# Kernel tuning notes

Hardware: AMD Instinct MI355X
Metric: run time of the kernel (lower is better)

## Reference

```python
import jax, jax.numpy as jnp
import numpy as np

B, D, NS, C, H = 4096, 1024, 16000, 1000, 256


def setup_inputs() -> dict:
    key = jax.random.key(0)
    ks = jax.random.split(key, 8)
    # L2-normalized image features (output of frozen CLIP encode_image + norm)
    q = jax.random.normal(ks[0], (B, D), jnp.float32)
    q = q / jnp.linalg.norm(q, axis=-1, keepdims=True)
    # zero-shot CLIP logits
    z = jax.random.normal(ks[1], (B, C), jnp.float32)
    # L2-normalized support/cache features
    keys = jax.random.normal(ks[2], (NS, D), jnp.float32)
    keys = keys / jnp.linalg.norm(keys, axis=-1, keepdims=True)
    # one-hot support labels
    labels = jax.random.randint(ks[3], (NS,), 0, C)
    values = jax.nn.one_hot(labels, C, dtype=jnp.float32)
    # gate MLP params (small init like nn.Linear default scale)
    fc1_w = jax.random.normal(ks[4], (H, D), jnp.float32) * 0.02
    fc1_b = jnp.zeros((H,), jnp.float32)
    fc2_w = jax.random.normal(ks[5], (2, H), jnp.float32) * 0.02
    fc2_b = jnp.zeros((2,), jnp.float32)
    post_scale = jnp.ones((1,), jnp.float32)
    return {"q": q, "z": z, "keys": keys, "values": values,
            "fc1_w": fc1_w, "fc1_b": fc1_b, "fc2_w": fc2_w, "fc2_b": fc2_b,
            "post_scale": post_scale}


def reference(q, z, keys, values, fc1_w, fc1_b, fc2_w, fc2_b, post_scale):
    # GateMLP: per-image alpha in (0,1), beta > 0
    x = jax.nn.relu(q @ fc1_w.T + fc1_b)            # [B, H]
    g = x @ fc2_w.T + fc2_b                          # [B, 2]
    alpha_hat = jax.nn.sigmoid(g[:, 0:1])            # [B, 1]
    beta = jax.nn.softplus(g[:, 1:2]) + 0.001        # [B, 1] (learn_beta=True)
    # cache logits: sim -> exp affinity -> label aggregation
    sim = q @ keys.T                                 # [B, Ns]
    affinity = jnp.exp(beta * sim)                   # [B, Ns]
    c = affinity @ values                            # [B, C]
    # gated convex fusion with zero-shot logits
    logits = ((1.0 - alpha_hat) * z + alpha_hat * c) * post_scale
    return (logits, alpha_hat, beta)
```

## Files before the change

kernel.cpp:

```cpp
#include <hip/hip_runtime.h>
#include <hip/hip_bf16.h>
#include <stdint.h>

#define B_  4096
#define D_  1024
#define NS_ 16000
#define C_  1000
#define H_  256
#define LBLK 4000
#define QCB  1024
#define KCB  4000
#define FCB  64
#define CONVB (QCB + KCB + FCB)
#define RSTRIDE 2048

typedef __attribute__((ext_vector_type(8))) short bf16x8;
typedef __attribute__((ext_vector_type(4))) float f32x4;
typedef __attribute__((ext_vector_type(16))) float f32x16;
typedef __attribute__((ext_vector_type(8))) int i32x8;

__device__ __forceinline__ unsigned short f2bf(float f) {
  union { float f; unsigned u; } v; v.f = f;
  unsigned u = v.u;
  u += 0x7FFF + ((u >> 16) & 1);
  return (unsigned short)(u >> 16);
}

__device__ __forceinline__ float bf2f(unsigned short h) {
  union { unsigned u; float f; } v; v.u = ((unsigned)h) << 16;
  return v.f;
}

__global__ void prep_kernel(const float4* __restrict__ q, const float4* __restrict__ keys,
                            const float4* __restrict__ fc1, const float* __restrict__ values,
                            ushort4* __restrict__ qb, int* __restrict__ q8,
                            int* __restrict__ keys8, ushort4* __restrict__ fc1b,
                            int* __restrict__ labels, int* __restrict__ hist) {
  const int bid = blockIdx.x;
  if (bid < QCB) {
    const size_t i0 = (size_t)bid * 1024 + threadIdx.x;
    #pragma unroll
    for (int k = 0; k < 4; ++k) {
      const size_t i = i0 + k * 256;
      float4 v = q[i];
      ushort4 r; r.x = f2bf(v.x); r.y = f2bf(v.y); r.z = f2bf(v.z); r.w = f2bf(v.w);
      qb[i] = r;
      int p = __builtin_amdgcn_cvt_pk_fp8_f32(v.x * 64.f, v.y * 64.f, 0, false);
      p     = __builtin_amdgcn_cvt_pk_fp8_f32(v.z * 64.f, v.w * 64.f, p, true);
      q8[i] = p;
    }
    return;
  }
  if (bid < QCB + KCB) {
    const size_t i0 = (size_t)(bid - QCB) * 1024 + threadIdx.x;
    #pragma unroll
    for (int k = 0; k < 4; ++k) {
      const size_t i = i0 + k * 256;
      float4 v = keys[i];
      int p = __builtin_amdgcn_cvt_pk_fp8_f32(v.x * 64.f, v.y * 64.f, 0, false);
      p     = __builtin_amdgcn_cvt_pk_fp8_f32(v.z * 64.f, v.w * 64.f, p, true);
      keys8[i] = p;
    }
    return;
  }
  if (bid < CONVB) {
    const size_t i0 = (size_t)(bid - QCB - KCB) * 1024 + threadIdx.x;
    #pragma unroll
    for (int k = 0; k < 4; ++k) {
      const size_t i = i0 + k * 256;
      float4 v = fc1[i];
      ushort4 r; r.x = f2bf(v.x); r.y = f2bf(v.y); r.z = f2bf(v.z); r.w = f2bf(v.w);
      fc1b[i] = r;
    }
    return;
  }
  const int s = (bid - CONVB) * 4 + (threadIdx.x >> 6);
  const int lane = threadIdx.x & 63;
  const float4* row = (const float4*)(values + (size_t)s * C_);
  int lab = -1;
  for (int j = lane; j < C_ / 4; j += 64) {
    float4 v = row[j];
    if (v.x > 0.5f) lab = j * 4 + 0;
    if (v.y > 0.5f) lab = j * 4 + 1;
    if (v.z > 0.5f) lab = j * 4 + 2;
    if (v.w > 0.5f) lab = j * 4 + 3;
    if (__ballot(lab >= 0)) break;
  }
  if (lab >= 0) { labels[s] = lab; atomicAdd(&hist[lab], 1); }
}

__global__ __launch_bounds__(1024) void sortpipe_kernel(
    const int* __restrict__ hist, const int* __restrict__ labels,
    int* __restrict__ sortidx, int* __restrict__ runid, int* __restrict__ labstart)
{
  __shared__ int sscan[1024];
  __shared__ int sboff[C_ + 1];
  __shared__ int scnt[C_];
  __shared__ unsigned short slab[NS_];
  __shared__ int stile[NS_ / 128];
  const int t = threadIdx.x;

  int v = (t < C_) ? hist[t] : 0;
  sscan[t] = v;
  if (t < C_) scnt[t] = 0;
  __syncthreads();
  for (int off = 1; off < 1024; off <<= 1) {
    int u = (t >= off) ? sscan[t - off] : 0;
    __syncthreads(); sscan[t] += u; __syncthreads();
  }
  if (t == 0) sboff[0] = 0;
  if (t < C_) sboff[t + 1] = sscan[t];
  __syncthreads();

  for (int s = t; s < NS_; s += 1024) {
    const int lab = labels[s];
    const int pos = sboff[lab] + atomicAdd(&scnt[lab], 1);
    sortidx[pos] = s;
    slab[pos] = (unsigned short)lab;
  }
  __syncthreads();

  const int c0 = t * 16;
  int flags[16]; int cnt = 0;
  if (c0 < NS_) {
    int prev = (c0 == 0) ? slab[0] : slab[c0 - 1];
    #pragma unroll
    for (int i = 0; i < 16; ++i) {
      const int l = slab[c0 + i];
      const int f = ((c0 + i) != 0) && (l != prev);
      flags[i] = f; cnt += f; prev = l;
    }
  }
  sscan[t] = cnt; __syncthreads();
  for (int off = 1; off < 1024; off <<= 1) {
    int u = (t >= off) ? sscan[t - off] : 0;
    __syncthreads(); sscan[t] += u; __syncthreads();
  }
  if (c0 < NS_ && (t & 7) == 0) stile[t >> 3] = (sscan[t] - cnt) + flags[0];
  __syncthreads();
  if (c0 < NS_) {
    int run = sscan[t] - cnt;
    const int base = (c0 >> 7) * 16 - stile[c0 >> 7];
    #pragma unroll
    for (int i = 0; i < 16; ++i) {
      run += flags[i];
      runid[c0 + i] = base + run;
    }
  }
  if (t == 0) runid[NS_] = (NS_ >> 7) * 16;
  __threadfence();
  __syncthreads();
  if (t <= C_) labstart[t] = runid[sboff[t]];
}

__global__ __launch_bounds__(256, 2) void gemmgate_kernel(
    const short* __restrict__ A, const short* __restrict__ Bm,
    const float* __restrict__ bias, const float* __restrict__ fc2_w,
    const float* __restrict__ fc2_b, float* __restrict__ ab)
{
  __shared__ short As[32 * 64];
  __shared__ short Bs[256 * 64];
  __shared__ float gred[4][32][2];

  const int tid  = threadIdx.x;
  const int wave = tid >> 6, lane = tid & 63;
  const int quad = lane >> 4, l16 = lane & 15;
  const int wn = wave;
  const int rstart = blockIdx.x * 32;

  f32x4 acc[2][4];
  #pragma unroll
  for (int i = 0; i < 2; ++i)
    #pragma unroll
    for (int j = 0; j < 4; ++j) acc[i][j] = (f32x4)0.f;

  const int r_  = (lane >> 3);
  const int kc_ = ((lane & 7) ^ r_) * 8;

  for (int kt = 0; kt < D_; kt += 64) {
    __syncthreads();
    {
      const int row = wave * 8 + r_;
      const short* gA = A + (size_t)(rstart + row) * D_ + kt + kc_;
      __builtin_amdgcn_global_load_lds(
          (const __attribute__((address_space(1))) void*)gA,
          (__attribute__((address_space(3))) void*)(As + wave * 512), 16, 0, 0);
    }
    #pragma unroll
    for (int i = 0; i < 8; ++i) {
      const int g = i * 4 + wave;
      const int row = g * 8 + r_;
      const short* gB = Bm + (size_t)row * D_ + kt + kc_;
      __builtin_amdgcn_global_load_lds(
          (const __attribute__((address_space(1))) void*)gB,
          (__attribute__((address_space(3))) void*)(Bs + g * 512), 16, 0, 0);
    }
    __syncthreads();
    #pragma unroll
    for (int ks = 0; ks < 64; ks += 32) {
      bf16x8 af[2], bfr[4];
      const int kb = (ks >> 3) + quad;
      #pragma unroll
      for (int mt = 0; mt < 2; ++mt) {
        const int row = mt * 16 + l16;
        af[mt] = *(const bf16x8*)(As + row * 64 + ((kb ^ (row & 7)) << 3));
      }
      #pragma unroll
      for (int nt = 0; nt < 4; ++nt) {
        const int row = wn * 64 + nt * 16 + l16;
        bfr[nt] = *(const bf16x8*)(Bs + row * 64 + ((kb ^ (row & 7)) << 3));
      }
      #pragma unroll
      for (int mt = 0; mt < 2; ++mt)
        #pragma unroll
        for (int nt = 0; nt < 4; ++nt)
          acc[mt][nt] = __builtin_amdgcn_mfma_f32_16x16x32_bf16(af[mt], bfr[nt], acc[mt][nt], 0, 0, 0);
    }
  }

  float g0p[2][4], g1p[2][4];
  #pragma unroll
  for (int mt = 0; mt < 2; ++mt)
    #pragma unroll
    for (int r = 0; r < 4; ++r) { g0p[mt][r] = 0.f; g1p[mt][r] = 0.f; }
  #pragma unroll
  for (int nt = 0; nt < 4; ++nt) {
    const int col = wn * 64 + nt * 16 + l16;
    const float bv = bias[col];
    const float w0 = fc2_w[col], w1 = fc2_w[H_ + col];
    #pragma unroll
    for (int mt = 0; mt < 2; ++mt)
      #pragma unroll
      for (int r = 0; r < 4; ++r) {
        float xv = acc[mt][nt][r] + bv;
        xv = xv > 0.f ? xv : 0.f;
        g0p[mt][r] += xv * w0;
        g1p[mt][r] += xv * w1;
      }
  }
  #pragma unroll
  for (int mt = 0; mt < 2; ++mt)
    #pragma unroll
    for (int r = 0; r < 4; ++r) {
      float a0 = g0p[mt][r], a1 = g1p[mt][r];
      #pragma unroll
      for (int off = 8; off > 0; off >>= 1) {
        a0 += __shfl_xor(a0, off);
        a1 += __shfl_xor(a1, off);
      }
      if (l16 == 0) {
        const int row = mt * 16 + quad * 4 + r;
        gred[wave][row][0] = a0;
        gred[wave][row][1] = a1;
      }
    }
  __syncthreads();
  if (tid < 32) {
    float g0 = gred[0][tid][0] + gred[1][tid][0] + gred[2][tid][0] + gred[3][tid][0] + fc2_b[0];
    float g1 = gred[0][tid][1] + gred[1][tid][1] + gred[2][tid][1] + gred[3][tid][1] + fc2_b[1];
    ab[rstart + tid]      = 1.f / (1.f + __expf(-g0));
    ab[B_ + rstart + tid] = fmaxf(g1, 0.f) + log1pf(__expf(-fabsf(g1))) + 0.001f;
  }
}

__device__ __forceinline__ i32x8 mx_frag(const char* base, int lrow, int kh, int sel) {
  const int c0 = kh * 4 + sel * 2;
  const int s = lrow & 7;
  const int4 lo = *(const int4*)(base + lrow * 128 + (((c0    ) ^ s) << 4));
  const int4 hi = *(const int4*)(base + lrow * 128 + (((c0 + 1) ^ s) << 4));
  i32x8 f;
  f[0] = lo.x; f[1] = lo.y; f[2] = lo.z; f[3] = lo.w;
  f[4] = hi.x; f[5] = hi.y; f[6] = hi.z; f[7] = hi.w;
  return f;
}

__global__ __launch_bounds__(256, 2) void mxgemm_kernel(
    const char* __restrict__ A8, const char* __restrict__ B8,
    const float* __restrict__ beta, float* __restrict__ partials,
    const int* __restrict__ sortidx, const int* __restrict__ runid)
{
  __shared__ __align__(16) char smem[32768];
  __shared__ float sbeta[128];
  __shared__ __align__(16) unsigned short Es[16 * 136];
  char* As = smem;
  char* Bs = smem + 16384;

  const int tid  = threadIdx.x;
  const int wave = tid >> 6, lane = tid & 63;
  const int sel  = lane >> 5, l32 = lane & 31;
  const int wm = wave >> 1, wn = wave & 1;

  const int sb  = (blockIdx.x & 7) * 500 + (blockIdx.x >> 3);
  const int rstart = (sb & 31) * 128;
  const int nstart = (sb >> 5) * 128;

  for (int i = tid; i < (16 * 136) / 2; i += 256) ((int*)Es)[i] = 0;
  if (tid < 128) sbeta[tid] = beta[rstart + tid];
  __syncthreads();
  if (tid < 128) Es[(runid[nstart + tid] & 15) * 136 + tid] = 0x3F80;

  const int srow_ = (lane >> 3);
  const int gch_  = (lane & 7) ^ srow_;

  int arow[4], brow[4];
  #pragma unroll
  for (int i = 0; i < 4; ++i) {
    const int row = wave * 32 + i * 8 + srow_;
    arow[i] = rstart + row;
    brow[i] = sortidx[nstart + row];
  }

  f32x16 acc[2][2];
  #pragma unroll
  for (int i = 0; i < 2; ++i)
    #pragma unroll
    for (int j = 0; j < 2; ++j) acc[i][j] = (f32x16)0.f;

  for (int kt = 0; kt < D_; kt += 128) {
    __syncthreads();
    #pragma unroll
    for (int i = 0; i < 4; ++i) {
      const char* gA = A8 + (size_t)arow[i] * D_ + kt + (gch_ << 4);
      const char* gB = B8 + (size_t)brow[i] * D_ + kt + (gch_ << 4);
      __builtin_amdgcn_global_load_lds(
          (const __attribute__((address_space(1))) void*)gA,
          (__attribute__((address_space(3))) void*)(As + wave * 4096 + i * 1024), 16, 0, 0);
      __builtin_amdgcn_global_load_lds(
          (const __attribute__((address_space(1))) void*)gB,
          (__attribute__((address_space(3))) void*)(Bs + wave * 4096 + i * 1024), 16, 0, 0);
    }
    __syncthreads();
    #pragma unroll
    for (int kh = 0; kh < 2; ++kh) {
      i32x8 a0 = mx_frag(As, wm * 64 +  0 + l32, kh, sel);
      i32x8 a1 = mx_frag(As, wm * 64 + 32 + l32, kh, sel);
      i32x8 b0 = mx_frag(Bs, wn * 64 +  0 + l32, kh, sel);
      i32x8 b1 = mx_frag(Bs, wn * 64 + 32 + l32, kh, sel);
      acc[0][0] = __builtin_amdgcn_mfma_scale_f32_32x32x64_f8f6f4(a0, b0, acc[0][0], 0, 0, 0, 121, 0, 121);
      acc[0][1] = __builtin_amdgcn_mfma_scale_f32_32x32x64_f8f6f4(a0, b1, acc[0][1], 0, 0, 0, 121, 0, 121);
      acc[1][0] = __builtin_amdgcn_mfma_scale_f32_32x32x64_f8f6f4(a1, b0, acc[1][0], 0, 0, 0, 121, 0, 121);
      acc[1][1] = __builtin_amdgcn_mfma_scale_f32_32x32x64_f8f6f4(a1, b1, acc[1][1], 0, 0, 0, 121, 0, 121);
    }
  }

  __syncthreads();
  unsigned short* tile = (unsigned short*)smem;
  #pragma unroll
  for (int mt = 0; mt < 2; ++mt) {
    #pragma unroll
    for (int nt = 0; nt < 2; ++nt) {
      const int col = wn * 64 + nt * 32 + l32;
      const int cc = col >> 3, cl = col & 7;
      #pragma unroll
      for (int r = 0; r < 16; ++r) {
        const int row = wm * 64 + mt * 32 + (r & 3) + 8 * (r >> 2) + 4 * sel;
        const float v = __expf(sbeta[row] * acc[mt][nt][r]);
        tile[row * 128 + (((cc ^ (row & 7)) << 3) | cl)] = f2bf(v);
      }
    }
  }
  __syncthreads();

  {
    const int quad = lane >> 4, l16 = lane & 15;
    const int rowb = wave * 32;
    f32x4 racc[2];
    racc[0] = (f32x4)0.f; racc[1] = (f32x4)0.f;
    #pragma unroll
    for (int kc = 0; kc < 4; ++kc) {
      const bf16x8 bfrag = *(const bf16x8*)(Es + l16 * 136 + kc * 32 + quad * 8);
      #pragma unroll
      for (int rg = 0; rg < 2; ++rg) {
        const int row = rowb + rg * 16 + l16;
        const int kch = kc * 4 + quad;
        const bf16x8 afrag = *(const bf16x8*)(tile + row * 128 + ((kch ^ (row & 7)) << 3));
        racc[rg] = __builtin_amdgcn_mfma_f32_16x16x32_bf16(afrag, bfrag, racc[rg], 0, 0, 0);
      }
    }
    const int tb = (nstart >> 7) * 16;
    #pragma unroll
    for (int rg = 0; rg < 2; ++rg) {
      #pragma unroll
      for (int r = 0; r < 4; ++r) {
        const int row = rowb + rg * 16 + quad * 4 + r;
        partials[(size_t)(rstart + row) * RSTRIDE + tb + l16] = racc[rg][r];
      }
    }
  }
}

__global__ __launch_bounds__(256) void reduce_kernel(
    const float* __restrict__ partials, const int* __restrict__ labstart,
    const float* __restrict__ z, const float* __restrict__ ps, float* __restrict__ out) {
  __shared__ __align__(16) float sp[RSTRIDE];
  __shared__ int sls[C_ + 1];
  const int b = blockIdx.x;
  const int t = threadIdx.x;
  for (int i = t; i <= C_; i += 256) sls[i] = labstart[i];
  const float4* p4 = (const float4*)(partials + (size_t)b * RSTRIDE);
  float4* s4 = (float4*)sp;
  for (int i = t; i < RSTRIDE / 4; i += 256) s4[i] = p4[i];
  __syncthreads();
  const float a  = out[(size_t)B_ * C_ + b];
  const float sc = ps[0];
  for (int lab = t; lab < C_; lab += 256) {
    float c = 0.f;
    for (int j = sls[lab]; j < sls[lab + 1]; ++j) c += sp[j];
    const size_t oi = (size_t)b * C_ + lab;
    out[oi] = ((1.f - a) * z[oi] + a * c) * sc;
  }
}

extern "C" void kernel_launch(void* const* d_in, const int* in_sizes, int n_in,
                              void* d_out, int out_size, void* d_ws, size_t ws_size,
                              hipStream_t stream) {
  const float* q          = (const float*)d_in[0];
  const float* z          = (const float*)d_in[1];
  const float* keys       = (const float*)d_in[2];
  const float* values     = (const float*)d_in[3];
  const float* fc1_w      = (const float*)d_in[4];
  const float* fc1_b      = (const float*)d_in[5];
  const float* fc2_w      = (const float*)d_in[6];
  const float* fc2_b      = (const float*)d_in[7];
  const float* post_scale = (const float*)d_in[8];
  float* out = (float*)d_out;

  char* ws = (char*)d_ws;
  short* qb        = (short*)(ws);
  char*  q8        = (char*) (ws +  8388608);
  char*  keys8     = (char*) (ws + 12582912);
  short* fc1b      = (short*)(ws + 28966912);
  int*   labels    = (int*)  (ws + 29491200);
  int*   hist      = (int*)  (ws + 33749504);
  int*   sortidx   = (int*)  (ws + 33761792);
  int*   runid     = (int*)  (ws + 33889792);
  int*   labstart  = (int*)  (ws + 33953808);
  float* partials  = (float*)(ws + 33959936);

  float* alpha = out + (size_t)B_ * C_;
  float* beta  = alpha + B_;

  hipMemsetAsync(hist, 0, 4096, stream);

  prep_kernel<<<CONVB + LBLK, 256, 0, stream>>>(
      (const float4*)q, (const float4*)keys, (const float4*)fc1_w, values,
      (ushort4*)qb, (int*)q8, (int*)keys8, (ushort4*)fc1b, labels, hist);

  sortpipe_kernel<<<1, 1024, 0, stream>>>(hist, labels, sortidx, runid, labstart);

  gemmgate_kernel<<<B_ / 32, 256, 0, stream>>>(qb, fc1b, fc1_b, fc2_w, fc2_b, alpha);

  mxgemm_kernel<<<4000, 256, 0, stream>>>(
      q8, keys8, beta, partials, sortidx, runid);

  reduce_kernel<<<B_, 256, 0, stream>>>(partials, labstart, z, post_scale, out);
}
```

Baseline: 324.3 us.

## Double-buffer LDS tiles in MX-FP8 GEMM and use a 2D grid

```diff
diff --git a/kernel.cpp b/kernel.cpp
--- a/kernel.cpp
+++ b/kernel.cpp
@@ -279,20 +279,16 @@
     const float* __restrict__ beta, float* __restrict__ partials,
     const int* __restrict__ sortidx, const int* __restrict__ runid)
 {
-  __shared__ __align__(16) char smem[32768];
+  __shared__ __align__(16) char smem[65536];
   __shared__ float sbeta[128];
   __shared__ __align__(16) unsigned short Es[16 * 136];
-  char* As = smem;
-  char* Bs = smem + 16384;
 
   const int tid  = threadIdx.x;
   const int wave = tid >> 6, lane = tid & 63;
   const int sel  = lane >> 5, l32 = lane & 31;
   const int wm = wave >> 1, wn = wave & 1;
-
-  const int sb  = (blockIdx.x & 7) * 500 + (blockIdx.x >> 3);
-  const int rstart = (sb & 31) * 128;
-  const int nstart = (sb >> 5) * 128;
+  const int rstart = blockIdx.x * 128;
+  const int nstart = blockIdx.y * 128;
 
   for (int i = tid; i < (16 * 136) / 2; i += 256) ((int*)Es)[i] = 0;
   if (tid < 128) sbeta[tid] = beta[rstart + tid];
@@ -316,34 +312,60 @@
     #pragma unroll
     for (int j = 0; j < 2; ++j) acc[i][j] = (f32x16)0.f;
 
-  for (int kt = 0; kt < D_; kt += 128) {
-    __syncthreads();
-    #pragma unroll
-    for (int i = 0; i < 4; ++i) {
-      const char* gA = A8 + (size_t)arow[i] * D_ + kt + (gch_ << 4);
-      const char* gB = B8 + (size_t)brow[i] * D_ + kt + (gch_ << 4);
-      __builtin_amdgcn_global_load_lds(
-          (const __attribute__((address_space(1))) void*)gA,
-          (__attribute__((address_space(3))) void*)(As + wave * 4096 + i * 1024), 16, 0, 0);
-      __builtin_amdgcn_global_load_lds(
-          (const __attribute__((address_space(1))) void*)gB,
-          (__attribute__((address_space(3))) void*)(Bs + wave * 4096 + i * 1024), 16, 0, 0);
-    }
-    __syncthreads();
-    #pragma unroll
-    for (int kh = 0; kh < 2; ++kh) {
-      i32x8 a0 = mx_frag(As, wm * 64 +  0 + l32, kh, sel);
-      i32x8 a1 = mx_frag(As, wm * 64 + 32 + l32, kh, sel);
-      i32x8 b0 = mx_frag(Bs, wn * 64 +  0 + l32, kh, sel);
-      i32x8 b1 = mx_frag(Bs, wn * 64 + 32 + l32, kh, sel);
-      acc[0][0] = __builtin_amdgcn_mfma_scale_f32_32x32x64_f8f6f4(a0, b0, acc[0][0], 0, 0, 0, 121, 0, 121);
-      acc[0][1] = __builtin_amdgcn_mfma_scale_f32_32x32x64_f8f6f4(a0, b1, acc[0][1], 0, 0, 0, 121, 0, 121);
-      acc[1][0] = __builtin_amdgcn_mfma_scale_f32_32x32x64_f8f6f4(a1, b0, acc[1][0], 0, 0, 0, 121, 0, 121);
-      acc[1][1] = __builtin_amdgcn_mfma_scale_f32_32x32x64_f8f6f4(a1, b1, acc[1][1], 0, 0, 0, 121, 0, 121);
-    }
-  }
-
-  __syncthreads();
+  __syncthreads();
+
+#define STAGE(BUF, KT)                                                              \
+  {                                                                                 \
+    char* As_ = smem + (BUF) * 32768;                                               \
+    char* Bs_ = As_ + 16384;                                                        \
+    _Pragma("unroll")                                                               \
+    for (int i = 0; i < 4; ++i) {                                                   \
+      const char* gA = A8 + (size_t)arow[i] * D_ + (KT) + (gch_ << 4);              \
+      const char* gB = B8 + (size_t)brow[i] * D_ + (KT) + (gch_ << 4);              \
+      __builtin_amdgcn_global_load_lds(                                             \
+          (const __attribute__((address_space(1))) void*)gA,                        \
+          (__attribute__((address_space(3))) void*)(As_ + wave * 4096 + i * 1024),  \
+          16, 0, 0);                                                                \
+      __builtin_amdgcn_global_load_lds(                                             \
+          (const __attribute__((address_space(1))) void*)gB,                        \
+          (__attribute__((address_space(3))) void*)(Bs_ + wave * 4096 + i * 1024),  \
+          16, 0, 0);                                                                \
+    }                                                                               \
+  }
+
+  STAGE(0, 0);
+  #pragma unroll
+  for (int t = 0; t < 8; ++t) {
+    if (t < 7) {
+      STAGE((t + 1) & 1, (t + 1) * 128);
+      asm volatile("s_waitcnt vmcnt(8)" ::: "memory");
+    } else {
+      asm volatile("s_waitcnt vmcnt(0)" ::: "memory");
+    }
+    __builtin_amdgcn_sched_barrier(0);
+    __builtin_amdgcn_s_barrier();
+    __builtin_amdgcn_sched_barrier(0);
+    {
+      const char* As_ = smem + (t & 1) * 32768;
+      const char* Bs_ = As_ + 16384;
+      #pragma unroll
+      for (int kh = 0; kh < 2; ++kh) {
+        i32x8 a0 = mx_frag(As_, wm * 64 +  0 + l32, kh, sel);
+        i32x8 a1 = mx_frag(As_, wm * 64 + 32 + l32, kh, sel);
+        i32x8 b0 = mx_frag(Bs_, wn * 64 +  0 + l32, kh, sel);
+        i32x8 b1 = mx_frag(Bs_, wn * 64 + 32 + l32, kh, sel);
+        acc[0][0] = __builtin_amdgcn_mfma_scale_f32_32x32x64_f8f6f4(a0, b0, acc[0][0], 0, 0, 0, 121, 0, 121);
+        acc[0][1] = __builtin_amdgcn_mfma_scale_f32_32x32x64_f8f6f4(a0, b1, acc[0][1], 0, 0, 0, 121, 0, 121);
+        acc[1][0] = __builtin_amdgcn_mfma_scale_f32_32x32x64_f8f6f4(a1, b0, acc[1][0], 0, 0, 0, 121, 0, 121);
+        acc[1][1] = __builtin_amdgcn_mfma_scale_f32_32x32x64_f8f6f4(a1, b1, acc[1][1], 0, 0, 0, 121, 0, 121);
+      }
+    }
+    __builtin_amdgcn_sched_barrier(0);
+    __builtin_amdgcn_s_barrier();
+    __builtin_amdgcn_sched_barrier(0);
+  }
+#undef STAGE
+
   unsigned short* tile = (unsigned short*)smem;
   #pragma unroll
   for (int mt = 0; mt < 2; ++mt) {
@@ -450,7 +472,7 @@
 
   gemmgate_kernel<<<B_ / 32, 256, 0, stream>>>(qb, fc1b, fc1_b, fc2_w, fc2_b, alpha);
 
-  mxgemm_kernel<<<4000, 256, 0, stream>>>(
+  mxgemm_kernel<<<dim3(B_ / 128, NS_ / 128), 256, 0, stream>>>(
       q8, keys8, beta, partials, sortidx, runid);
 
   reduce_kernel<<<B_, 256, 0, stream>>>(partials, labstart, z, post_scale, out);
```

After: 346.5 us. +6.9%, slower.

## Merge sort pipeline and gate GEMM into one launch; use 2D grid for mxgemm

Applied to the files above, without the earlier changes.

```diff
diff --git a/kernel.cpp b/kernel.cpp
--- a/kernel.cpp
+++ b/kernel.cpp
@@ -89,58 +89,186 @@
   if (lab >= 0) { labels[s] = lab; atomicAdd(&hist[lab], 1); }
 }
 
-__global__ __launch_bounds__(1024) void sortpipe_kernel(
+union MidShared {
+  struct {
+    short As[32 * 64];
+    short Bs[256 * 64];
+    float gred[4][32][2];
+  } g;
+  struct {
+    int sscan[1024];
+    int sboff[C_ + 1];
+    int scnt[C_];
+    unsigned short slab[NS_];
+    int stile[NS_ / 128];
+  } s;
+};
+
+__global__ __launch_bounds__(1024) void midpipe_kernel(
+    const short* __restrict__ A, const short* __restrict__ Bm,
+    const float* __restrict__ bias, const float* __restrict__ fc2_w,
+    const float* __restrict__ fc2_b, float* __restrict__ ab,
     const int* __restrict__ hist, const int* __restrict__ labels,
     int* __restrict__ sortidx, int* __restrict__ runid, int* __restrict__ labstart)
 {
-  __shared__ int sscan[1024];
-  __shared__ int sboff[C_ + 1];
-  __shared__ int scnt[C_];
-  __shared__ unsigned short slab[NS_];
-  __shared__ int stile[NS_ / 128];
-  const int t = threadIdx.x;
-
+  __shared__ MidShared u;
+  const int tid = threadIdx.x;
+
+  if (blockIdx.x < B_ / 32) {
+    short* As = u.g.As;
+    short* Bs = u.g.Bs;
+    const bool act = tid < 256;
+    const int wave = (tid >> 6) & 3, lane = tid & 63;
+    const int quad = lane >> 4, l16 = lane & 15;
+    const int wn = wave;
+    const int rstart = blockIdx.x * 32;
+
+    f32x4 acc[2][4];
+    #pragma unroll
+    for (int i = 0; i < 2; ++i)
+      #pragma unroll
+      for (int j = 0; j < 4; ++j) acc[i][j] = (f32x4)0.f;
+
+    const int r_  = (lane >> 3);
+    const int kc_ = ((lane & 7) ^ r_) * 8;
+
+    for (int kt = 0; kt < D_; kt += 64) {
+      __syncthreads();
+      if (act) {
+        {
+          const int row = wave * 8 + r_;
+          const short* gA = A + (size_t)(rstart + row) * D_ + kt + kc_;
+          __builtin_amdgcn_global_load_lds(
+              (const __attribute__((address_space(1))) void*)gA,
+              (__attribute__((address_space(3))) void*)(As + wave * 512), 16, 0, 0);
+        }
+        #pragma unroll
+        for (int i = 0; i < 8; ++i) {
+          const int g = i * 4 + wave;
+          const int row = g * 8 + r_;
+          const short* gB = Bm + (size_t)row * D_ + kt + kc_;
+          __builtin_amdgcn_global_load_lds(
+              (const __attribute__((address_space(1))) void*)gB,
+              (__attribute__((address_space(3))) void*)(Bs + g * 512), 16, 0, 0);
+        }
+      }
+      __syncthreads();
+      if (act) {
+        #pragma unroll
+        for (int ks = 0; ks < 64; ks += 32) {
+          bf16x8 af[2], bfr[4];
+          const int kb = (ks >> 3) + quad;
+          #pragma unroll
+          for (int mt = 0; mt < 2; ++mt) {
+            const int row = mt * 16 + l16;
+            af[mt] = *(const bf16x8*)(As + row * 64 + ((kb ^ (row & 7)) << 3));
+          }
+          #pragma unroll
+          for (int nt = 0; nt < 4; ++nt) {
+            const int row = wn * 64 + nt * 16 + l16;
+            bfr[nt] = *(const bf16x8*)(Bs + row * 64 + ((kb ^ (row & 7)) << 3));
+          }
+          #pragma unroll
+          for (int mt = 0; mt < 2; ++mt)
+            #pragma unroll
+            for (int nt = 0; nt < 4; ++nt)
+              acc[mt][nt] = __builtin_amdgcn_mfma_f32_16x16x32_bf16(af[mt], bfr[nt], acc[mt][nt], 0, 0, 0);
+        }
+      }
+    }
+
+    if (act) {
+      float g0p[2][4], g1p[2][4];
+      #pragma unroll
+      for (int mt = 0; mt < 2; ++mt)
+        #pragma unroll
+        for (int r = 0; r < 4; ++r) { g0p[mt][r] = 0.f; g1p[mt][r] = 0.f; }
+      #pragma unroll
+      for (int nt = 0; nt < 4; ++nt) {
+        const int col = wn * 64 + nt * 16 + l16;
+        const float bv = bias[col];
+        const float w0 = fc2_w[col], w1 = fc2_w[H_ + col];
+        #pragma unroll
+        for (int mt = 0; mt < 2; ++mt)
+          #pragma unroll
+          for (int r = 0; r < 4; ++r) {
+            float xv = acc[mt][nt][r] + bv;
+            xv = xv > 0.f ? xv : 0.f;
+            g0p[mt][r] += xv * w0;
+            g1p[mt][r] += xv * w1;
+          }
+      }
+      #pragma unroll
+      for (int mt = 0; mt < 2; ++mt)
+        #pragma unroll
+        for (int r = 0; r < 4; ++r) {
+          float a0 = g0p[mt][r], a1 = g1p[mt][r];
+          #pragma unroll
+          for (int off = 8; off > 0; off >>= 1) {
+            a0 += __shfl_xor(a0, off);
+            a1 += __shfl_xor(a1, off);
+          }
+          if (l16 == 0) {
+            const int row = mt * 16 + quad * 4 + r;
+            u.g.gred[wave][row][0] = a0;
+            u.g.gred[wave][row][1] = a1;
+          }
+        }
+    }
+    __syncthreads();
+    if (tid < 32) {
+      float g0 = u.g.gred[0][tid][0] + u.g.gred[1][tid][0] + u.g.gred[2][tid][0] +
+                 u.g.gred[3][tid][0] + fc2_b[0];
+      float g1 = u.g.gred[0][tid][1] + u.g.gred[1][tid][1] + u.g.gred[2][tid][1] +
+                 u.g.gred[3][tid][1] + fc2_b[1];
+      ab[rstart + tid]      = 1.f / (1.f + __expf(-g0));
+      ab[B_ + rstart + tid] = fmaxf(g1, 0.f) + log1pf(__expf(-fabsf(g1))) + 0.001f;
+    }
+    return;
+  }
+
+  const int t = tid;
   int v = (t < C_) ? hist[t] : 0;
-  sscan[t] = v;
-  if (t < C_) scnt[t] = 0;
+  u.s.sscan[t] = v;
+  if (t < C_) u.s.scnt[t] = 0;
   __syncthreads();
   for (int off = 1; off < 1024; off <<= 1) {
-    int u = (t >= off) ? sscan[t - off] : 0;
-    __syncthreads(); sscan[t] += u; __syncthreads();
-  }
-  if (t == 0) sboff[0] = 0;
-  if (t < C_) sboff[t + 1] = sscan[t];
+    int w = (t >= off) ? u.s.sscan[t - off] : 0;
+    __syncthreads(); u.s.sscan[t] += w; __syncthreads();
+  }
+  if (t == 0) u.s.sboff[0] = 0;
+  if (t < C_) u.s.sboff[t + 1] = u.s.sscan[t];
   __syncthreads();
 
   for (int s = t; s < NS_; s += 1024) {
     const int lab = labels[s];
-    const int pos = sboff[lab] + atomicAdd(&scnt[lab], 1);
+    const int pos = u.s.sboff[lab] + atomicAdd(&u.s.scnt[lab], 1);
     sortidx[pos] = s;
-    slab[pos] = (unsigned short)lab;
+    u.s.slab[pos] = (unsigned short)lab;
   }
   __syncthreads();
 
   const int c0 = t * 16;
   int flags[16]; int cnt = 0;
   if (c0 < NS_) {
-    int prev = (c0 == 0) ? slab[0] : slab[c0 - 1];
+    int prev = (c0 == 0) ? u.s.slab[0] : u.s.slab[c0 - 1];
     #pragma unroll
     for (int i = 0; i < 16; ++i) {
-      const int l = slab[c0 + i];
+      const int l = u.s.slab[c0 + i];
       const int f = ((c0 + i) != 0) && (l != prev);
       flags[i] = f; cnt += f; prev = l;
     }
   }
-  sscan[t] = cnt; __syncthreads();
+  u.s.sscan[t] = cnt; __syncthreads();
   for (int off = 1; off < 1024; off <<= 1) {
-    int u = (t >= off) ? sscan[t - off] : 0;
-    __syncthreads(); sscan[t] += u; __syncthreads();
-  }
-  if (c0 < NS_ && (t & 7) == 0) stile[t >> 3] = (sscan[t] - cnt) + flags[0];
+    int w = (t >= off) ? u.s.sscan[t - off] : 0;
+    __syncthreads(); u.s.sscan[t] += w; __syncthreads();
+  }
+  if (c0 < NS_ && (t & 7) == 0) u.s.stile[t >> 3] = (u.s.sscan[t] - cnt) + flags[0];
   __syncthreads();
   if (c0 < NS_) {
-    int run = sscan[t] - cnt;
-    const int base = (c0 >> 7) * 16 - stile[c0 >> 7];
+    int run = u.s.sscan[t] - cnt;
+    const int base = (c0 >> 7) * 16 - u.s.stile[c0 >> 7];
     #pragma unroll
     for (int i = 0; i < 16; ++i) {
       run += flags[i];
@@ -150,117 +278,7 @@
   if (t == 0) runid[NS_] = (NS_ >> 7) * 16;
   __threadfence();
   __syncthreads();
-  if (t <= C_) labstart[t] = runid[sboff[t]];
-}
-
-__global__ __launch_bounds__(256, 2) void gemmgate_kernel(
-    const short* __restrict__ A, const short* __restrict__ Bm,
-    const float* __restrict__ bias, const float* __restrict__ fc2_w,
-    const float* __restrict__ fc2_b, float* __restrict__ ab)
-{
-  __shared__ short As[32 * 64];
-  __shared__ short Bs[256 * 64];
-  __shared__ float gred[4][32][2];
-
-  const int tid  = threadIdx.x;
-  const int wave = tid >> 6, lane = tid & 63;
-  const int quad = lane >> 4, l16 = lane & 15;
-  const int wn = wave;
-  const int rstart = blockIdx.x * 32;
-
-  f32x4 acc[2][4];
-  #pragma unroll
-  for (int i = 0; i < 2; ++i)
-    #pragma unroll
-    for (int j = 0; j < 4; ++j) acc[i][j] = (f32x4)0.f;
-
-  const int r_  = (lane >> 3);
-  const int kc_ = ((lane & 7) ^ r_) * 8;
-
-  for (int kt = 0; kt < D_; kt += 64) {
-    __syncthreads();
-    {
-      const int row = wave * 8 + r_;
-      const short* gA = A + (size_t)(rstart + row) * D_ + kt + kc_;
-      __builtin_amdgcn_global_load_lds(
-          (const __attribute__((address_space(1))) void*)gA,
-          (__attribute__((address_space(3))) void*)(As + wave * 512), 16, 0, 0);
-    }
-    #pragma unroll
-    for (int i = 0; i < 8; ++i) {
-      const int g = i * 4 + wave;
-      const int row = g * 8 + r_;
-      const short* gB = Bm + (size_t)row * D_ + kt + kc_;
-      __builtin_amdgcn_global_load_lds(
-          (const __attribute__((address_space(1))) void*)gB,
-          (__attribute__((address_space(3))) void*)(Bs + g * 512), 16, 0, 0);
-    }
-    __syncthreads();
-    #pragma unroll
-    for (int ks = 0; ks < 64; ks += 32) {
-      bf16x8 af[2], bfr[4];
-      const int kb = (ks >> 3) + quad;
-      #pragma unroll
-      for (int mt = 0; mt < 2; ++mt) {
-        const int row = mt * 16 + l16;
-        af[mt] = *(const bf16x8*)(As + row * 64 + ((kb ^ (row & 7)) << 3));
-      }
-      #pragma unroll
-      for (int nt = 0; nt < 4; ++nt) {
-        const int row = wn * 64 + nt * 16 + l16;
-        bfr[nt] = *(const bf16x8*)(Bs + row * 64 + ((kb ^ (row & 7)) << 3));
-      }
-      #pragma unroll
-      for (int mt = 0; mt < 2; ++mt)
-        #pragma unroll
-        for (int nt = 0; nt < 4; ++nt)
-          acc[mt][nt] = __builtin_amdgcn_mfma_f32_16x16x32_bf16(af[mt], bfr[nt], acc[mt][nt], 0, 0, 0);
-    }
-  }
-
-  float g0p[2][4], g1p[2][4];
-  #pragma unroll
-  for (int mt = 0; mt < 2; ++mt)
-    #pragma unroll
-    for (int r = 0; r < 4; ++r) { g0p[mt][r] = 0.f; g1p[mt][r] = 0.f; }
-  #pragma unroll
-  for (int nt = 0; nt < 4; ++nt) {
-    const int col = wn * 64 + nt * 16 + l16;
-    const float bv = bias[col];
-    const float w0 = fc2_w[col], w1 = fc2_w[H_ + col];
-    #pragma unroll
-    for (int mt = 0; mt < 2; ++mt)
-      #pragma unroll
-      for (int r = 0; r < 4; ++r) {
-        float xv = acc[mt][nt][r] + bv;
-        xv = xv > 0.f ? xv : 0.f;
-        g0p[mt][r] += xv * w0;
-        g1p[mt][r] += xv * w1;
-      }
-  }
-  #pragma unroll
-  for (int mt = 0; mt < 2; ++mt)
-    #pragma unroll
-    for (int r = 0; r < 4; ++r) {
-      float a0 = g0p[mt][r], a1 = g1p[mt][r];
-      #pragma unroll
-      for (int off = 8; off > 0; off >>= 1) {
-        a0 += __shfl_xor(a0, off);
-        a1 += __shfl_xor(a1, off);
-      }
-      if (l16 == 0) {
-        const int row = mt * 16 + quad * 4 + r;
-        gred[wave][row][0] = a0;
-        gred[wave][row][1] = a1;
-      }
-    }
-  __syncthreads();
-  if (tid < 32) {
-    float g0 = gred[0][tid][0] + gred[1][tid][0] + gred[2][tid][0] + gred[3][tid][0] + fc2_b[0];
-    float g1 = gred[0][tid][1] + gred[1][tid][1] + gred[2][tid][1] + gred[3][tid][1] + fc2_b[1];
-    ab[rstart + tid]      = 1.f / (1.f + __expf(-g0));
-    ab[B_ + rstart + tid] = fmaxf(g1, 0.f) + log1pf(__expf(-fabsf(g1))) + 0.001f;
-  }
+  if (t <= C_) labstart[t] = runid[u.s.sboff[t]];
 }
 
 __device__ __forceinline__ i32x8 mx_frag(const char* base, int lrow, int kh, int sel) {
@@ -289,10 +307,8 @@
   const int wave = tid >> 6, lane = tid & 63;
   const int sel  = lane >> 5, l32 = lane & 31;
   const int wm = wave >> 1, wn = wave & 1;
-
-  const int sb  = (blockIdx.x & 7) * 500 + (blockIdx.x >> 3);
-  const int rstart = (sb & 31) * 128;
-  const int nstart = (sb >> 5) * 128;
+  const int rstart = blockIdx.x * 128;
+  const int nstart = blockIdx.y * 128;
 
   for (int i = tid; i < (16 * 136) / 2; i += 256) ((int*)Es)[i] = 0;
   if (tid < 128) sbeta[tid] = beta[rstart + tid];
@@ -446,11 +462,10 @@
       (const float4*)q, (const float4*)keys, (const float4*)fc1_w, values,
       (ushort4*)qb, (int*)q8, (int*)keys8, (ushort4*)fc1b, labels, hist);
 
-  sortpipe_kernel<<<1, 1024, 0, stream>>>(hist, labels, sortidx, runid, labstart);
-
-  gemmgate_kernel<<<B_ / 32, 256, 0, stream>>>(qb, fc1b, fc1_b, fc2_w, fc2_b, alpha);
-
-  mxgemm_kernel<<<4000, 256, 0, stream>>>(
+  midpipe_kernel<<<B_ / 32 + 1, 1024, 0, stream>>>(
+      qb, fc1b, fc1_b, fc2_w, fc2_b, alpha, hist, labels, sortidx, runid, labstart);
+
+  mxgemm_kernel<<<dim3(B_ / 128, NS_ / 128), 256, 0, stream>>>(
       q8, keys8, beta, partials, sortidx, runid);
 
   reduce_kernel<<<B_, 256, 0, stream>>>(partials, labstart, z, post_scale, out);
```

After: 320.7 us. About the same (-1.1%).
